# Optimization experiments

Hardware: AMD Instinct MI355X
Metric: run time of the kernel (lower is better)

Reference implementation:

```python
import jax, jax.numpy as jnp
import numpy as np

N, B, D = 8, 4096, 1024
LOG_2PI = np.float32(np.log(2.0 * np.pi))


def setup_inputs() -> dict:
    key = jax.random.key(0)
    k1, k2 = jax.random.split(key)
    means = jax.random.normal(k1, (N, B, D), dtype=jnp.float32)
    logsigmas = jax.random.normal(k2, (N, B, D), dtype=jnp.float32)
    return {"means": means, "logsigmas": logsigmas}


def reference(means, logsigmas):
    # Sequential product of diagonal Gaussians.
    # Original builds DxD diag matrices + MVN log_prob; mathematically this is
    # purely elementwise over D plus a sum for the log-normalizer.
    m0, lv0 = means[0], logsigmas[0]
    lz0 = jnp.zeros(means.shape[1], dtype=means.dtype)

    def step(carry, inp):
        m1, lv1, lz = carry          # prior mean, log-variance, accumulated log_z
        m2, lv2 = inp                # next component
        v1 = jnp.exp(lv1)
        v2 = jnp.exp(lv2)
        iv1 = 1.0 / v1
        iv2 = 1.0 / v2
        cvar = 1.0 / (iv1 + iv2)              # combined variance (diag of C)
        cmean = cvar * (m1 * iv1 + m2 * iv2)  # combined mean
        s = v1 + v2 + 1e-6                    # covariance of the normalizer Gaussian
        # MVN(m2, diag(s)).log_prob(m1) == sum of univariate normal log-pdfs
        log_z = -0.5 * jnp.sum((m1 - m2) ** 2 / s + jnp.log(s) + LOG_2PI, axis=-1)
        return (cmean, jnp.log(cvar), lz + log_z), None

    (post_mean, post_logvar, log_z_total), _ = jax.lax.scan(
        step, (m0, lv0, lz0), (means[1:], logsigmas[1:])
    )
    return post_mean, post_logvar, log_z_total
```

## Files before the change

kernel.cpp:

```cpp
#include <hip/hip_runtime.h>
#include <math.h>

#define NN 8
#define BB 4096
#define DD 1024
#define LOG_2PI 1.8378770664093453f

__global__ __launch_bounds__(256) void mpc_kernel(
    const float* __restrict__ means,
    const float* __restrict__ logsig,
    float* __restrict__ out_mean,
    float* __restrict__ out_logvar,
    float* __restrict__ out_logz)
{
    const int b = blockIdx.x;
    const int t = threadIdx.x;
    const size_t rowoff = (size_t)b * DD + (size_t)t * 4;
    const size_t plane = (size_t)BB * DD;

    float4 M[NN], L[NN];
#pragma unroll
    for (int n = 0; n < NN; ++n) {
        M[n] = *(const float4*)(means + (size_t)n * plane + rowoff);
        L[n] = *(const float4*)(logsig + (size_t)n * plane + rowoff);
    }

    float m1[4], v1[4], iv1[4];
    {
        float m[4] = {M[0].x, M[0].y, M[0].z, M[0].w};
        float l[4] = {L[0].x, L[0].y, L[0].z, L[0].w};
#pragma unroll
        for (int j = 0; j < 4; ++j) {
            m1[j]  = m[j];
            v1[j]  = __expf(l[j]);
            iv1[j] = __expf(-l[j]);
        }
    }

    float z = 0.0f;

#pragma unroll
    for (int n = 1; n < NN; ++n) {
        float m2[4] = {M[n].x, M[n].y, M[n].z, M[n].w};
        float l2[4] = {L[n].x, L[n].y, L[n].z, L[n].w};
#pragma unroll
        for (int j = 0; j < 4; ++j) {
            float v2  = __expf(l2[j]);
            float iv2 = __expf(-l2[j]);
            float s   = v1[j] + v2 + 1e-6f;
            float diff = m1[j] - m2[j];
            z += diff * diff * __builtin_amdgcn_rcpf(s) + __logf(s);
            float iv_new = iv1[j] + iv2;
            float cvar   = __builtin_amdgcn_rcpf(iv_new);
            m1[j]  = cvar * (m1[j] * iv1[j] + m2[j] * iv2);
            v1[j]  = cvar;
            iv1[j] = iv_new;
        }
    }

    float4 om = make_float4(m1[0], m1[1], m1[2], m1[3]);
    float4 ol = make_float4(__logf(v1[0]), __logf(v1[1]),
                            __logf(v1[2]), __logf(v1[3]));
    *(float4*)(out_mean + rowoff)   = om;
    *(float4*)(out_logvar + rowoff) = ol;

#pragma unroll
    for (int o = 32; o > 0; o >>= 1)
        z += __shfl_down(z, o, 64);

    __shared__ float sz[4];
    const int wave = t >> 6;
    const int lane = t & 63;
    if (lane == 0) sz[wave] = z;
    __syncthreads();
    if (t == 0) {
        float total = sz[0] + sz[1] + sz[2] + sz[3];
        out_logz[b] = -0.5f * (total + (float)((NN - 1) * DD) * LOG_2PI);
    }
}

extern "C" void kernel_launch(void* const* d_in, const int* in_sizes, int n_in,
                              void* d_out, int out_size, void* d_ws, size_t ws_size,
                              hipStream_t stream) {
    const float* means  = (const float*)d_in[0];
    const float* logsig = (const float*)d_in[1];
    float* out = (float*)d_out;
    float* out_mean   = out;
    float* out_logvar = out + (size_t)BB * DD;
    float* out_logz   = out + 2 * (size_t)BB * DD;
    mpc_kernel<<<BB, 256, 0, stream>>>(means, logsig, out_mean, out_logvar, out_logz);
}
```

Baseline: 293.3 us.

## Stream inputs via global_load_lds with staged vmcnt waits in single-wave blocks

Each row is now split across four single-wave blocks. Every wave issues its eight mean and logsigma loads straight into LDS through global_load_lds. Each scan step waits only on the vmcnt for its own plane, so compute on early components overlaps the loads still in flight for later ones. The per-row log_z reduction becomes an atomicAdd of partials into a buffer zeroed by a memset. This adds an extra memset launch and atomics, and it relies on the LDS-direct load ordering matching the hand-counted vmcnt values.

```diff
diff --git a/kernel.cpp b/kernel.cpp
--- a/kernel.cpp
+++ b/kernel.cpp
@@ -4,32 +4,47 @@
 #define NN 8
 #define BB 4096
 #define DD 1024
+#define CHUNK 256
 #define LOG_2PI 1.8378770664093453f
 
-__global__ __launch_bounds__(256) void mpc_kernel(
+
+#define GLOAD_LDS16(g, l)                                                  \
+    __builtin_amdgcn_global_load_lds(                                      \
+        (const __attribute__((address_space(1))) unsigned int*)(g),        \
+        (__attribute__((address_space(3))) unsigned int*)(l), 16, 0, 0)
+
+#define WAITVM(imm) asm volatile("s_waitcnt vmcnt(" #imm ")" ::: "memory")
+
+__global__ __launch_bounds__(64) void mpc_kernel(
     const float* __restrict__ means,
     const float* __restrict__ logsig,
     float* __restrict__ out_mean,
     float* __restrict__ out_logvar,
     float* __restrict__ out_logz)
 {
-    const int b = blockIdx.x;
-    const int t = threadIdx.x;
-    const size_t rowoff = (size_t)b * DD + (size_t)t * 4;
+    __shared__ float smem[16 * CHUNK];
+
+    const int blk  = blockIdx.x;
+    const int b    = blk >> 2;
+    const int c    = blk & 3;
+    const int lane = threadIdx.x;
+    const size_t base  = (size_t)b * DD + (size_t)c * CHUNK + (size_t)lane * 4;
     const size_t plane = (size_t)BB * DD;
 
-    float4 M[NN], L[NN];
 #pragma unroll
     for (int n = 0; n < NN; ++n) {
-        M[n] = *(const float4*)(means + (size_t)n * plane + rowoff);
-        L[n] = *(const float4*)(logsig + (size_t)n * plane + rowoff);
+        GLOAD_LDS16(means  + (size_t)n * plane + base, &smem[(2 * n + 0) * CHUNK]);
+        GLOAD_LDS16(logsig + (size_t)n * plane + base, &smem[(2 * n + 1) * CHUNK]);
     }
 
     float m1[4], v1[4], iv1[4];
+    float z = 0.0f;
+    WAITVM(14);
     {
-        float m[4] = {M[0].x, M[0].y, M[0].z, M[0].w};
-        float l[4] = {L[0].x, L[0].y, L[0].z, L[0].w};
-#pragma unroll
+        float4 mm = *(const float4*)&smem[0 * CHUNK + lane * 4];
+        float4 ll = *(const float4*)&smem[1 * CHUNK + lane * 4];
+        float m[4] = {mm.x, mm.y, mm.z, mm.w};
+        float l[4] = {ll.x, ll.y, ll.z, ll.w};
         for (int j = 0; j < 4; ++j) {
             m1[j]  = m[j];
             v1[j]  = __expf(l[j]);
@@ -37,45 +52,47 @@
         }
     }
 
-    float z = 0.0f;
+#define STEP(n, imm) do {                                                   \
+        WAITVM(imm);                                                        \
+        float4 mm = *(const float4*)&smem[(2 * (n) + 0) * CHUNK + lane * 4];\
+        float4 ll = *(const float4*)&smem[(2 * (n) + 1) * CHUNK + lane * 4];\
+        float m2[4] = {mm.x, mm.y, mm.z, mm.w};                             \
+        float l2[4] = {ll.x, ll.y, ll.z, ll.w};                             \
+        for (int j = 0; j < 4; ++j) {                                       \
+            float v2  = __expf(l2[j]);                                      \
+            float iv2 = __expf(-l2[j]);                                     \
+            float s   = v1[j] + v2 + 1e-6f;                                 \
+            float diff = m1[j] - m2[j];                                     \
+            z += diff * diff * __builtin_amdgcn_rcpf(s) + __logf(s);        \
+            float iv_new = iv1[j] + iv2;                                    \
+            float cvar   = __builtin_amdgcn_rcpf(iv_new);                   \
+            m1[j]  = cvar * (m1[j] * iv1[j] + m2[j] * iv2);                 \
+            v1[j]  = cvar;                                                  \
+            iv1[j] = iv_new;                                                \
+        }                                                                   \
+    } while (0)
 
-#pragma unroll
-    for (int n = 1; n < NN; ++n) {
-        float m2[4] = {M[n].x, M[n].y, M[n].z, M[n].w};
-        float l2[4] = {L[n].x, L[n].y, L[n].z, L[n].w};
-#pragma unroll
-        for (int j = 0; j < 4; ++j) {
-            float v2  = __expf(l2[j]);
-            float iv2 = __expf(-l2[j]);
-            float s   = v1[j] + v2 + 1e-6f;
-            float diff = m1[j] - m2[j];
-            z += diff * diff * __builtin_amdgcn_rcpf(s) + __logf(s);
-            float iv_new = iv1[j] + iv2;
-            float cvar   = __builtin_amdgcn_rcpf(iv_new);
-            m1[j]  = cvar * (m1[j] * iv1[j] + m2[j] * iv2);
-            v1[j]  = cvar;
-            iv1[j] = iv_new;
-        }
-    }
+    STEP(1, 12);
+    STEP(2, 10);
+    STEP(3, 8);
+    STEP(4, 6);
+    STEP(5, 4);
+    STEP(6, 2);
+    STEP(7, 0);
+#undef STEP
 
     float4 om = make_float4(m1[0], m1[1], m1[2], m1[3]);
     float4 ol = make_float4(__logf(v1[0]), __logf(v1[1]),
                             __logf(v1[2]), __logf(v1[3]));
-    *(float4*)(out_mean + rowoff)   = om;
-    *(float4*)(out_logvar + rowoff) = ol;
+    *(float4*)(out_mean + base)   = om;
+    *(float4*)(out_logvar + base) = ol;
 
 #pragma unroll
     for (int o = 32; o > 0; o >>= 1)
         z += __shfl_down(z, o, 64);
-
-    __shared__ float sz[4];
-    const int wave = t >> 6;
-    const int lane = t & 63;
-    if (lane == 0) sz[wave] = z;
-    __syncthreads();
-    if (t == 0) {
-        float total = sz[0] + sz[1] + sz[2] + sz[3];
-        out_logz[b] = -0.5f * (total + (float)((NN - 1) * DD) * LOG_2PI);
+    if (lane == 0) {
+        float partial = -0.5f * z - 0.125f * (float)((NN - 1) * DD) * LOG_2PI;
+        atomicAdd(out_logz + b, partial);
     }
 }
 
@@ -88,5 +105,6 @@
     float* out_mean   = out;
     float* out_logvar = out + (size_t)BB * DD;
     float* out_logz   = out + 2 * (size_t)BB * DD;
-    mpc_kernel<<<BB, 256, 0, stream>>>(means, logsig, out_mean, out_logvar, out_logz);
+    hipMemsetAsync(out_logz, 0, BB * sizeof(float), stream);
+    mpc_kernel<<<BB * 4, 64, 0, stream>>>(means, logsig, out_mean, out_logvar, out_logz);
 }
```

Measured after the change: 289.3 us. No clear change (-1.4%).
